# Performance work log

Measured on AMD Instinct MI355X. Metric: run time of the kernel, lower is better.

Reference implementation:

```python
import jax, jax.numpy as jnp
import numpy as np

B, T, H, F, K, NB, MAXL = 32, 512, 512, 512, 3, 256, 2048


def _conv1d(x, w, b, pad):
    # x: [B,T,Cin], w: [K,Cin,Cout] -> [B,T,Cout]
    y = jax.lax.conv_general_dilated(x, w, window_strides=(1,), padding=[(pad, pad)],
                                     dimension_numbers=('NWC', 'WIO', 'NWC'))
    return y + b


def _layernorm(x, g, b):
    m = jnp.mean(x, axis=-1, keepdims=True)
    v = jnp.mean((x - m) ** 2, axis=-1, keepdims=True)
    return (x - m) * jax.lax.rsqrt(v + 1e-5) * g + b


def _variance_predictor(x, mask, cw1, cb1, g1, b1, cw2, cb2, g2, b2, lw, lb, k):
    # ConvNorm(k, pad=(k-1)//2) -> ReLU -> LN -> ConvNorm(k, pad=1) -> ReLU -> LN -> Linear(F,1)
    h = _layernorm(jax.nn.relu(_conv1d(x, cw1, cb1, (k - 1) // 2)), g1, b1)
    h = _layernorm(jax.nn.relu(_conv1d(h, cw2, cb2, 1)), g2, b2)
    out = h @ lw + lb  # [B,T]
    return jnp.where(mask, 0.0, out)


def setup_inputs() -> dict:
    key = jax.random.key(0)
    ks = jax.random.split(key, 12)
    s = 0.02
    inp = {
        'x': jax.random.normal(ks[0], (B, T, H), jnp.float32),
        'src_mask': jnp.zeros((B, T), jnp.bool_),
        'duration': jax.random.randint(ks[1], (B, T), 0, 8),
        'pitch_target': jax.random.normal(ks[2], (B, T), jnp.float32),
        'energy_target': jax.random.normal(ks[3], (B, T), jnp.float32),
        # stacked predictor params: index 0=duration, 1=pitch, 2=energy
        'conv1_w': jax.random.normal(ks[4], (3, K, H, F), jnp.float32) * s,
        'conv1_b': jnp.zeros((3, F), jnp.float32),
        'ln1_g': jnp.ones((3, F), jnp.float32),
        'ln1_b': jnp.zeros((3, F), jnp.float32),
        'conv2_w': jax.random.normal(ks[5], (3, K, F, F), jnp.float32) * s,
        'conv2_b': jnp.zeros((3, F), jnp.float32),
        'ln2_g': jnp.ones((3, F), jnp.float32),
        'ln2_b': jnp.zeros((3, F), jnp.float32),
        'lin_w': jax.random.normal(ks[6], (3, F), jnp.float32) * s,
        'lin_b': jnp.zeros((3,), jnp.float32),
        'pitch_bins': jnp.linspace(-3.0, 3.0, NB - 1, dtype=jnp.float32),
        'energy_bins': jnp.linspace(-3.0, 3.0, NB - 1, dtype=jnp.float32),
        'pitch_table': jax.random.normal(ks[7], (NB, H), jnp.float32) * s,
        'energy_table': jax.random.normal(ks[8], (NB, H), jnp.float32) * s,
        'max_len': MAXL,
    }
    return inp


def reference(x, src_mask, duration, pitch_target, energy_target,
              conv1_w, conv1_b, ln1_g, ln1_b, conv2_w, conv2_b, ln2_g, ln2_b,
              lin_w, lin_b, pitch_bins, energy_bins, pitch_table, energy_table, max_len):
    k = conv1_w.shape[1]

    def vp(i, inp):
        return _variance_predictor(inp, src_mask, conv1_w[i], conv1_b[i], ln1_g[i], ln1_b[i],
                                   conv2_w[i], conv2_b[i], ln2_g[i], ln2_b[i], lin_w[i], lin_b[i], k)

    log_duration_pred = vp(0, x)
    # pitch: predict, bucketize target, add embedding (training path with targets)
    pitch_pred = vp(1, x)
    p_idx = jnp.searchsorted(pitch_bins, pitch_target)  # torch.bucketize
    x = x + pitch_table[p_idx]
    # energy on pitch-conditioned features
    energy_pred = vp(2, x)
    e_idx = jnp.searchsorted(energy_bins, energy_target)
    x = x + energy_table[e_idx]

    # LengthRegulator: expand each phoneme vec duration[b,i] times, pad to max_len
    dur = jnp.where(src_mask, 0, duration)
    cum = jnp.cumsum(dur, axis=1)                 # [B,T]
    mel_len = jnp.minimum(cum[:, -1], max_len)    # [B]
    frames = jnp.arange(max_len)
    idx = jax.vmap(lambda c: jnp.searchsorted(c, frames, side='right'))(cum)
    idx = jnp.clip(idx, 0, x.shape[1] - 1)        # [B,max_len]
    x_out = jnp.take_along_axis(x, idx[:, :, None], axis=1)  # [B,max_len,H]
    mel_mask = frames[None, :] >= mel_len[:, None]
    x_out = jnp.where(mel_mask[:, :, None], 0.0, x_out)
    return x_out, log_duration_pred, pitch_pred, energy_pred, mel_len, mel_mask
```

## Files before the change

kernel.cpp:

```cpp
#include <hip/hip_runtime.h>
#include <hip/hip_bf16.h>

typedef unsigned short ushort_t;
typedef unsigned int uint_t;
typedef __attribute__((ext_vector_type(8))) short bf16x8;
typedef __attribute__((ext_vector_type(4))) float f32x4;

#define NB_T 512
#define NB_B 32
#define NB_M (NB_B * NB_T)
#define KDIM 1536
#define MAXL 2048
#define EPI_STRIDE 144

__device__ __forceinline__ ushort_t f2bf(float f) {
  __hip_bfloat16 h = __float2bfloat16(f);
  return *reinterpret_cast<ushort_t*>(&h);
}
__device__ __forceinline__ float bf2f(ushort_t u) {
  __hip_bfloat16 h;
  *reinterpret_cast<ushort_t*>(&h) = u;
  return __bfloat162float(h);
}
__device__ __forceinline__ uint_t pack2(float a, float b) {
  return (uint_t)f2bf(a) | ((uint_t)f2bf(b) << 16);
}
__device__ __forceinline__ void gload_lds16(const void* g, void* l) {
  __builtin_amdgcn_global_load_lds((const __attribute__((address_space(1))) void*)g,
                                   (__attribute__((address_space(3))) void*)l, 16, 0, 0);
}

__global__ __launch_bounds__(256) void k_wt(const float* __restrict__ w1, const float* __restrict__ w2,
                                            ushort_t* __restrict__ wt1, ushort_t* __restrict__ wt2) {
  __shared__ float tile[64][65];
  int g = blockIdx.y;
  const float* wsrc;
  ushort_t* wdst;
  if (g < 9) { wsrc = w1; wdst = wt1; } else { wsrc = w2; wdst = wt2; g -= 9; }
  const int p = g / 3, kk = g % 3;
  const int ot = (blockIdx.x & 7) * 64;
  const int it = (blockIdx.x >> 3) * 64;
  const int tx = threadIdx.x & 63;
  const int ty = threadIdx.x >> 6;
  const float* src = wsrc + (size_t)g * 512 * 512;
  #pragma unroll
  for (int r = ty; r < 64; r += 4)
    tile[r][tx] = src[(size_t)(it + r) * 512 + ot + tx];
  __syncthreads();
  #pragma unroll
  for (int r = ty; r < 64; r += 4)
    wdst[((size_t)(p * 512 + ot + r)) * KDIM + kk * 512 + it + tx] = f2bf(tile[tx][r]);
}

__global__ __launch_bounds__(512) void k_cum(const int* __restrict__ dur, const unsigned char* __restrict__ mask,
                                             int* __restrict__ cum, float* __restrict__ mel_len_out) {
  __shared__ int s[512];
  const int b = blockIdx.x, t = threadIdx.x;
  int d = mask[b * NB_T + t] ? 0 : dur[b * NB_T + t];
  s[t] = d;
  __syncthreads();
  for (int off = 1; off < 512; off <<= 1) {
    int v = (t >= off) ? s[t - off] : 0;
    __syncthreads();
    s[t] += v;
    __syncthreads();
  }
  cum[b * NB_T + t] = s[t];
  if (t == 0) {
    int ml = s[511]; ml = ml < MAXL ? ml : MAXL;
    mel_len_out[b] = (float)ml;
  }
}

__global__ __launch_bounds__(256) void k_prep(const float* __restrict__ x,
                                              const float* __restrict__ pt, const float* __restrict__ et,
                                              const float* __restrict__ pb, const float* __restrict__ eb,
                                              const float* __restrict__ ptab, const float* __restrict__ etab,
                                              ushort_t* __restrict__ xb_pad, ushort_t* __restrict__ x2pad,
                                              ushort_t* __restrict__ lnp2, ushort_t* __restrict__ x3b) {
  const int rp = blockIdx.x;
  const int b = rp / 514, j = rp % 514;
  const int tid = threadIdx.x;
  if (j == 0 || j == 513) {
    ((uint_t*)(xb_pad + (size_t)rp * 512))[tid] = 0u;
    ((uint_t*)(x2pad + (size_t)rp * 512))[tid] = 0u;
    ((uint_t*)(lnp2 + (size_t)rp * 512))[tid] = 0u;
    return;
  }
  const int m = b * NB_T + j - 1;
  float v = pt[m];
  int lo = 0, hi = 255;
  while (lo < hi) { int mid = (lo + hi) >> 1; if (pb[mid] < v) lo = mid + 1; else hi = mid; }
  const int pi = lo;
  v = et[m]; lo = 0; hi = 255;
  while (lo < hi) { int mid = (lo + hi) >> 1; if (eb[mid] < v) lo = mid + 1; else hi = mid; }
  const int ei = lo;

  const float2 xv = ((const float2*)(x + (size_t)m * 512))[tid];
  const float2 pv = ((const float2*)(ptab + (size_t)pi * 512))[tid];
  const float2 ev = ((const float2*)(etab + (size_t)ei * 512))[tid];
  ((uint_t*)(xb_pad + (size_t)rp * 512))[tid] = pack2(xv.x, xv.y);
  const float ax = xv.x + pv.x, ay = xv.y + pv.y;
  ((uint_t*)(x2pad + (size_t)rp * 512))[tid] = pack2(ax, ay);
  ((uint_t*)(x3b + (size_t)m * 512))[tid] = pack2(ax + ev.x, ay + ev.y);
}

__global__ __launch_bounds__(256) void k_gemm(const ushort_t* __restrict__ A0,
                                              const ushort_t* __restrict__ A1,
                                              const ushort_t* __restrict__ A2,
                                              const ushort_t* __restrict__ Wt,
                                              const float* __restrict__ bias,
                                              ushort_t* __restrict__ H) {
  __shared__ short smem[18432];
  const int tid = threadIdx.x;
  const int lane = tid & 63, wid = tid >> 6;

  const int h = blockIdx.x;
  const int logical = (h & 7) * 192 + (h >> 3);
  const int pred = logical >> 9;
  const int tile = logical & 511;
  const int mt = tile >> 2, nt = tile & 3;
  const int m0 = mt * 128, n0 = nt * 128;
  const int b = m0 >> 9, t0 = m0 & 511;
  const long Arow0 = (long)b * 514 + t0 + 1;

  const ushort_t* Ap = (pred == 0) ? A0 : ((pred == 1) ? A1 : A2);
  const ushort_t* Wp = Wt + (size_t)pred * 512 * KDIM;
  const float* bp = bias + pred * 512;
  ushort_t* Hp = H + (size_t)pred * NB_M * 512;

  const int subr = lane >> 2;
  const int ioff = (lane & 3) * 8;
  const int wr = wid >> 1, wc = wid & 1;
  const int lr = lane & 15, kg = lane >> 4;

  f32x4 acc[4][4];
  #pragma unroll
  for (int i = 0; i < 4; ++i)
    #pragma unroll
    for (int j = 0; j < 4; ++j) acc[i][j] = (f32x4)0.f;

  auto STAGE = [&](int kk, int buf) {
    const int dt = (kk >> 4) - 1;
    const int i0 = (kk & 15) << 5;
    short* la = &smem[buf * 8192];
    short* lb = &smem[buf * 8192 + 4096];
    #pragma unroll
    for (int q = 0; q < 2; ++q) {
      const int chunk = wid * 2 + q;
      const int r = chunk * 16 + subr;
      gload_lds16(Ap + (size_t)(Arow0 + r + dt) * 512 + i0 + ioff, &la[chunk * 512]);
      gload_lds16(Wp + (size_t)(n0 + r) * KDIM + kk * 32 + ioff, &lb[chunk * 512]);
    }
  };

  STAGE(0, 0);
  __syncthreads();
  int buf = 0;
  for (int kk = 0; kk < 48; ++kk) {
    if (kk < 47) STAGE(kk + 1, buf ^ 1);
    const short* la = &smem[buf * 8192];
    const short* lb = &smem[buf * 8192 + 4096];
    bf16x8 af[4], bfv[4];
    #pragma unroll
    for (int fi = 0; fi < 4; ++fi)
      af[fi] = *(const bf16x8*)&la[(wr * 64 + fi * 16 + lr) * 32 + kg * 8];
    #pragma unroll
    for (int fj = 0; fj < 4; ++fj)
      bfv[fj] = *(const bf16x8*)&lb[(wc * 64 + fj * 16 + lr) * 32 + kg * 8];
    #pragma unroll
    for (int fi = 0; fi < 4; ++fi)
      #pragma unroll
      for (int fj = 0; fj < 4; ++fj)
        acc[fi][fj] = __builtin_amdgcn_mfma_f32_16x16x32_bf16(af[fi], bfv[fj], acc[fi][fj], 0, 0, 0);
    __syncthreads();
    buf ^= 1;
  }

  float bvv[4];
  #pragma unroll
  for (int fj = 0; fj < 4; ++fj) bvv[fj] = bp[n0 + wc * 64 + fj * 16 + lr];
  #pragma unroll
  for (int fi = 0; fi < 4; ++fi) {
    const int rowb = wr * 64 + fi * 16 + kg * 4;
    #pragma unroll
    for (int fj = 0; fj < 4; ++fj) {
      const int col = wc * 64 + fj * 16 + lr;
      #pragma unroll
      for (int r = 0; r < 4; ++r) {
        float v = acc[fi][fj][r] + bvv[fj];
        v = v > 0.f ? v : 0.f;
        smem[(rowb + r) * EPI_STRIDE + col] = (short)f2bf(v);
      }
    }
  }
  __syncthreads();
  #pragma unroll
  for (int s = 0; s < 8; ++s) {
    const int chunk = tid + s * 256;
    const int row = chunk >> 4, c8 = (chunk & 15) * 8;
    bf16x8 vv = *(const bf16x8*)&smem[row * EPI_STRIDE + c8];
    *(bf16x8*)(Hp + (size_t)(m0 + row) * 512 + n0 + c8) = vv;
  }
}

__global__ __launch_bounds__(256) void k_ln_mid(const ushort_t* __restrict__ Hh,
                                                const float* __restrict__ g, const float* __restrict__ bb,
                                                ushort_t* __restrict__ lnp0, ushort_t* __restrict__ lnp1,
                                                ushort_t* __restrict__ lnp2) {
  const int rr = blockIdx.x * 4 + (threadIdx.x >> 6);
  const int pred = rr >> 14, m = rr & (NB_M - 1);
  const int lane = threadIdx.x & 63;
  const float* gp = g + pred * 512;
  const float* bp = bb + pred * 512;
  ushort_t* dst = (pred == 0) ? lnp0 : ((pred == 1) ? lnp1 : lnp2);
  bf16x8 v = *(const bf16x8*)(Hh + (size_t)rr * 512 + lane * 8);
  float xv[8];
  float s = 0.f;
  #pragma unroll
  for (int j = 0; j < 8; ++j) { xv[j] = bf2f((ushort_t)v[j]); s += xv[j]; }
  #pragma unroll
  for (int mm = 32; mm >= 1; mm >>= 1) s += __shfl_xor(s, mm, 64);
  const float mean = s * (1.f / 512.f);
  float vs = 0.f;
  #pragma unroll
  for (int j = 0; j < 8; ++j) { float d = xv[j] - mean; vs += d * d; }
  #pragma unroll
  for (int mm = 32; mm >= 1; mm >>= 1) vs += __shfl_xor(vs, mm, 64);
  const float rstd = rsqrtf(vs * (1.f / 512.f) + 1e-5f);
  const float4 g0 = ((const float4*)(gp + lane * 8))[0];
  const float4 g1 = ((const float4*)(gp + lane * 8))[1];
  const float4 b0 = ((const float4*)(bp + lane * 8))[0];
  const float4 b1 = ((const float4*)(bp + lane * 8))[1];
  const float gg[8] = {g0.x, g0.y, g0.z, g0.w, g1.x, g1.y, g1.z, g1.w};
  const float bv[8] = {b0.x, b0.y, b0.z, b0.w, b1.x, b1.y, b1.z, b1.w};
  bf16x8 o;
  #pragma unroll
  for (int j = 0; j < 8; ++j) o[j] = (short)f2bf((xv[j] - mean) * rstd * gg[j] + bv[j]);
  const int bidx = m >> 9, t = m & 511;
  *(bf16x8*)(dst + ((size_t)(bidx * 514 + t + 1)) * 512 + lane * 8) = o;
}

__global__ __launch_bounds__(256) void k_ln_fin(const ushort_t* __restrict__ Hh,
                                                const float* __restrict__ g, const float* __restrict__ bb,
                                                const float* __restrict__ lw, const float* __restrict__ lbp,
                                                const unsigned char* __restrict__ mask,
                                                float* __restrict__ outp) {
  const int rr = blockIdx.x * 4 + (threadIdx.x >> 6);
  const int pred = rr >> 14, m = rr & (NB_M - 1);
  const int lane = threadIdx.x & 63;
  const float* gp = g + pred * 512;
  const float* bp = bb + pred * 512;
  const float* wp = lw + pred * 512;
  bf16x8 v = *(const bf16x8*)(Hh + (size_t)rr * 512 + lane * 8);
  float xv[8];
  float s = 0.f;
  #pragma unroll
  for (int j = 0; j < 8; ++j) { xv[j] = bf2f((ushort_t)v[j]); s += xv[j]; }
  #pragma unroll
  for (int mm = 32; mm >= 1; mm >>= 1) s += __shfl_xor(s, mm, 64);
  const float mean = s * (1.f / 512.f);
  float vs = 0.f;
  #pragma unroll
  for (int j = 0; j < 8; ++j) { float d = xv[j] - mean; vs += d * d; }
  #pragma unroll
  for (int mm = 32; mm >= 1; mm >>= 1) vs += __shfl_xor(vs, mm, 64);
  const float rstd = rsqrtf(vs * (1.f / 512.f) + 1e-5f);
  const float4 g0 = ((const float4*)(gp + lane * 8))[0];
  const float4 g1 = ((const float4*)(gp + lane * 8))[1];
  const float4 b0 = ((const float4*)(bp + lane * 8))[0];
  const float4 b1 = ((const float4*)(bp + lane * 8))[1];
  const float4 w0 = ((const float4*)(wp + lane * 8))[0];
  const float4 w1 = ((const float4*)(wp + lane * 8))[1];
  const float gg[8] = {g0.x, g0.y, g0.z, g0.w, g1.x, g1.y, g1.z, g1.w};
  const float bv[8] = {b0.x, b0.y, b0.z, b0.w, b1.x, b1.y, b1.z, b1.w};
  const float ww[8] = {w0.x, w0.y, w0.z, w0.w, w1.x, w1.y, w1.z, w1.w};
  float dot = 0.f;
  #pragma unroll
  for (int j = 0; j < 8; ++j) dot += ((xv[j] - mean) * rstd * gg[j] + bv[j]) * ww[j];
  #pragma unroll
  for (int mm = 32; mm >= 1; mm >>= 1) dot += __shfl_xor(dot, mm, 64);
  if (lane == 0) {
    float val = dot + lbp[pred];
    if (mask[m]) val = 0.f;
    outp[pred * NB_M + m] = val;
  }
}

__global__ __launch_bounds__(256) void k_regulate(const ushort_t* __restrict__ x3b, const int* __restrict__ cum,
                                                  float* __restrict__ xout, float* __restrict__ mmask) {
  __shared__ int c[512];
  const int blk = blockIdx.x;
  const int b = blk >> 5, chunk = blk & 31;
  const int tid = threadIdx.x, lane = tid & 63, w = tid >> 6;
  c[tid] = cum[b * NB_T + tid];
  c[tid + 256] = cum[b * NB_T + tid + 256];
  __syncthreads();
  int ml = c[511]; ml = ml < MAXL ? ml : MAXL;
  const int f0 = chunk * 64 + w * 16;
  for (int i = 0; i < 16; ++i) {
    const int f = f0 + i;
    float o[8] = {0.f, 0.f, 0.f, 0.f, 0.f, 0.f, 0.f, 0.f};
    if (f < ml) {
      int lo = 0, hi = 512;
      while (lo < hi) { int mid = (lo + hi) >> 1; if (c[mid] <= f) lo = mid + 1; else hi = mid; }
      if (lo > 511) lo = 511;
      bf16x8 vv = *(const bf16x8*)(x3b + ((size_t)(b * NB_T + lo)) * 512 + lane * 8);
      #pragma unroll
      for (int j = 0; j < 8; ++j) o[j] = bf2f((ushort_t)vv[j]);
    }
    float* dst = xout + ((size_t)(b * MAXL + f)) * 512 + lane * 8;
    ((float4*)dst)[0] = make_float4(o[0], o[1], o[2], o[3]);
    ((float4*)dst)[1] = make_float4(o[4], o[5], o[6], o[7]);
    if (lane == 0) mmask[b * MAXL + f] = (f >= ml) ? 1.0f : 0.0f;
  }
}

extern "C" void kernel_launch(void* const* d_in, const int* in_sizes, int n_in,
                              void* d_out, int out_size, void* d_ws, size_t ws_size,
                              hipStream_t stream) {
  const float* x        = (const float*)d_in[0];
  const unsigned char* src_mask = (const unsigned char*)d_in[1];
  const int* duration   = (const int*)d_in[2];
  const float* pitch_t  = (const float*)d_in[3];
  const float* energy_t = (const float*)d_in[4];
  const float* conv1_w  = (const float*)d_in[5];
  const float* conv1_b  = (const float*)d_in[6];
  const float* ln1_g    = (const float*)d_in[7];
  const float* ln1_b    = (const float*)d_in[8];
  const float* conv2_w  = (const float*)d_in[9];
  const float* conv2_b  = (const float*)d_in[10];
  const float* ln2_g    = (const float*)d_in[11];
  const float* ln2_b    = (const float*)d_in[12];
  const float* lin_w    = (const float*)d_in[13];
  const float* lin_b    = (const float*)d_in[14];
  const float* pbins    = (const float*)d_in[15];
  const float* ebins    = (const float*)d_in[16];
  const float* ptab     = (const float*)d_in[17];
  const float* etab     = (const float*)d_in[18];

  char* ws = (char*)d_ws;
  ushort_t* wt1    = (ushort_t*)(ws + 0);
  ushort_t* wt2    = (ushort_t*)(ws + 4718592);
  ushort_t* xb_pad = (ushort_t*)(ws + 9437184);
  ushort_t* x2pad  = (ushort_t*)(ws + 26279936);
  ushort_t* lnp2   = (ushort_t*)(ws + 43122688);
  ushort_t* hbuf   = (ushort_t*)(ws + 59965440);
  ushort_t* x3b    = (ushort_t*)(ws + 110297088);
  int*      cum    = (int*)     (ws + 127074304);

  float* out      = (float*)d_out;
  float* o_xout   = out;
  float* o_preds  = out + 33554432;
  float* o_mellen = o_preds + 3 * NB_M;
  float* o_mmask  = o_mellen + 32;

  k_cum<<<NB_B, 512, 0, stream>>>(duration, src_mask, cum, o_mellen);
  k_wt<<<dim3(64, 18), 256, 0, stream>>>(conv1_w, conv2_w, wt1, wt2);
  k_prep<<<NB_B * 514, 256, 0, stream>>>(x, pitch_t, energy_t, pbins, ebins, ptab, etab,
                                         xb_pad, x2pad, lnp2, x3b);

  k_gemm<<<1536, 256, 0, stream>>>(xb_pad, xb_pad, x2pad, wt1, conv1_b, hbuf);
  k_ln_mid<<<3 * NB_M / 4, 256, 0, stream>>>(hbuf, ln1_g, ln1_b, xb_pad, x2pad, lnp2);
  k_gemm<<<1536, 256, 0, stream>>>(xb_pad, x2pad, lnp2, wt2, conv2_b, hbuf);
  k_ln_fin<<<3 * NB_M / 4, 256, 0, stream>>>(hbuf, ln2_g, ln2_b, lin_w, lin_b, src_mask, o_preds);

  k_regulate<<<1024, 256, 0, stream>>>(x3b, cum, o_xout, o_mmask);
}
```

Measured before the change: 496.0 us.

## Rework conv GEMM to 256x256 tiles with swizzled LDS and phased prefetch

Replaces the 128x128, 4-wave GEMM with 256x256 tiles using 8 waves and 128KB of dynamic LDS, a K-step of 64, and an XOR-swizzled LDS layout to avoid bank conflicts. Prefetch of the next stage is split into four parts interleaved with MFMA phases, using explicit barriers, setprio and vmcnt waits. The epilogue now writes bf16 directly to global instead of staging through LDS. The larger tile is meant to raise operand reuse and MFMA density, at the cost of one block per CU, only 384 blocks, and uncoalesced 2-byte epilogue stores.

Result: no change. 502.6 us (+1.3%).

```diff
diff --git a/kernel.cpp b/kernel.cpp
--- a/kernel.cpp
+++ b/kernel.cpp
@@ -11,7 +11,6 @@
 #define NB_M (NB_B * NB_T)
 #define KDIM 1536
 #define MAXL 2048
-#define EPI_STRIDE 144
 
 __device__ __forceinline__ ushort_t f2bf(float f) {
   __hip_bfloat16 h = __float2bfloat16(f);
@@ -105,22 +104,24 @@
   ((uint_t*)(x3b + (size_t)m * 512))[tid] = pack2(ax + ev.x, ay + ev.y);
 }
 
-__global__ __launch_bounds__(256) void k_gemm(const ushort_t* __restrict__ A0,
-                                              const ushort_t* __restrict__ A1,
-                                              const ushort_t* __restrict__ A2,
-                                              const ushort_t* __restrict__ Wt,
-                                              const float* __restrict__ bias,
-                                              ushort_t* __restrict__ H) {
-  __shared__ short smem[18432];
+__global__ __launch_bounds__(512, 1) void k_gemm(const ushort_t* __restrict__ A0,
+                                                 const ushort_t* __restrict__ A1,
+                                                 const ushort_t* __restrict__ A2,
+                                                 const ushort_t* __restrict__ Wt,
+                                                 const float* __restrict__ bias,
+                                                 ushort_t* __restrict__ H) {
+  extern __shared__ char smem[];
   const int tid = threadIdx.x;
   const int lane = tid & 63, wid = tid >> 6;
-
-  const int h = blockIdx.x;
-  const int logical = (h & 7) * 192 + (h >> 3);
-  const int pred = logical >> 9;
-  const int tile = logical & 511;
-  const int mt = tile >> 2, nt = tile & 3;
-  const int m0 = mt * 128, n0 = nt * 128;
+  const int wr = wid >> 2, wc = wid & 3;
+  const int l15 = lane & 15, l4 = lane >> 4;
+
+  const int bid = blockIdx.x;
+  const int logical = (bid & 7) * 48 + (bid >> 3);
+  const int pred = logical >> 7;
+  const int tl = logical & 127;
+  const int mt = tl >> 1, nt = tl & 1;
+  const int m0 = mt << 8, n0 = nt << 8;
   const int b = m0 >> 9, t0 = m0 & 511;
   const long Arow0 = (long)b * 514 + t0 + 1;
 
@@ -129,78 +130,100 @@
   const float* bp = bias + pred * 512;
   ushort_t* Hp = H + (size_t)pred * NB_M * 512;
 
-  const int subr = lane >> 2;
-  const int ioff = (lane & 3) * 8;
-  const int wr = wid >> 1, wc = wid & 1;
-  const int lr = lane & 15, kg = lane >> 4;
-
-  f32x4 acc[4][4];
-  #pragma unroll
-  for (int i = 0; i < 4; ++i)
+  f32x4 acc[8][4];
+  #pragma unroll
+  for (int i = 0; i < 8; ++i)
     #pragma unroll
     for (int j = 0; j < 4; ++j) acc[i][j] = (f32x4)0.f;
 
-  auto STAGE = [&](int kk, int buf) {
-    const int dt = (kk >> 4) - 1;
-    const int i0 = (kk & 15) << 5;
-    short* la = &smem[buf * 8192];
-    short* lb = &smem[buf * 8192 + 4096];
+  auto STAGE = [&](int jt, int bbuf, int part) {
+    const int h = part & 1;
+    const bool isB = part >= 2;
+    const int tap = jt >> 3;
+    const int kin = (jt & 7) << 6;
     #pragma unroll
     for (int q = 0; q < 2; ++q) {
-      const int chunk = wid * 2 + q;
-      const int r = chunk * 16 + subr;
-      gload_lds16(Ap + (size_t)(Arow0 + r + dt) * 512 + i0 + ioff, &la[chunk * 512]);
-      gload_lds16(Wp + (size_t)(n0 + r) * KDIM + kk * 32 + ioff, &lb[chunk * 512]);
+      const int Ll = q * 8192 + tid * 16;
+      const int Pl = Ll ^ (((Ll >> 9) & 1) << 5);
+      const int row = Pl >> 7;
+      const int kel = (Pl & 127) >> 1;
+      char* ldsb = smem + bbuf * 65536 + (isB ? 32768 : 0) + h * 16384
+                 + q * 8192 + (tid & ~63) * 16;
+      const ushort_t* src;
+      if (isB) src = Wp + (size_t)(n0 + h * 128 + row) * KDIM + jt * 64 + kel;
+      else     src = Ap + (size_t)(Arow0 + h * 128 + row + (tap - 1)) * 512 + kin + kel;
+      gload_lds16(src, ldsb);
     }
   };
-
-  STAGE(0, 0);
-  __syncthreads();
-  int buf = 0;
-  for (int kk = 0; kk < 48; ++kk) {
-    if (kk < 47) STAGE(kk + 1, buf ^ 1);
-    const short* la = &smem[buf * 8192];
-    const short* lb = &smem[buf * 8192 + 4096];
-    bf16x8 af[4], bfv[4];
+  auto LDA = [&](int bbuf, int fr, int ks) -> bf16x8 {
+    const int R = wr * 128 + fr * 16 + l15;
+    const int kb = (ks * 64 + l4 * 16) ^ (((R >> 2) & 1) << 5);
+    return *(const bf16x8*)(smem + bbuf * 65536 + R * 128 + kb);
+  };
+  auto LDB = [&](int bbuf, int fc, int ks) -> bf16x8 {
+    const int R = wc * 64 + fc * 16 + l15;
+    const int kb = (ks * 64 + l4 * 16) ^ (((R >> 2) & 1) << 5);
+    return *(const bf16x8*)(smem + bbuf * 65536 + 32768 + R * 128 + kb);
+  };
+
+  #pragma unroll
+  for (int part = 0; part < 4; ++part) STAGE(0, 0, part);
+  #pragma unroll
+  for (int part = 0; part < 4; ++part) STAGE(1, 1, part);
+  asm volatile("s_waitcnt vmcnt(8)" ::: "memory");
+  __builtin_amdgcn_s_barrier();
+
+  for (int s = 0; s < 24; ++s) {
+    const int bb = s & 1;
+    bf16x8 bF[4][2];
     #pragma unroll
-    for (int fi = 0; fi < 4; ++fi)
-      af[fi] = *(const bf16x8*)&la[(wr * 64 + fi * 16 + lr) * 32 + kg * 8];
+    for (int p = 0; p < 4; ++p) {
+      bf16x8 aF[2][2];
+      #pragma unroll
+      for (int i = 0; i < 2; ++i)
+        #pragma unroll
+        for (int ks = 0; ks < 2; ++ks)
+          aF[i][ks] = LDA(bb, 2 * p + i, ks);
+      if (p == 0) {
+        #pragma unroll
+        for (int fc = 0; fc < 4; ++fc)
+          #pragma unroll
+          for (int ks = 0; ks < 2; ++ks)
+            bF[fc][ks] = LDB(bb, fc, ks);
+      }
+      if (s >= 1 && s <= 22) STAGE(s + 1, bb ^ 1, p);
+      __builtin_amdgcn_s_barrier();
+      __builtin_amdgcn_s_setprio(1);
+      #pragma unroll
+      for (int ks = 0; ks < 2; ++ks)
+        #pragma unroll
+        for (int i = 0; i < 2; ++i)
+          #pragma unroll
+          for (int fc = 0; fc < 4; ++fc)
+            acc[2 * p + i][fc] = __builtin_amdgcn_mfma_f32_16x16x32_bf16(
+                aF[i][ks], bF[fc][ks], acc[2 * p + i][fc], 0, 0, 0);
+      __builtin_amdgcn_s_setprio(0);
+      if (p == 3) asm volatile("s_waitcnt vmcnt(0)" ::: "memory");
+      __builtin_amdgcn_s_barrier();
+    }
+  }
+
+  float bvv[4];
+  #pragma unroll
+  for (int fc = 0; fc < 4; ++fc) bvv[fc] = bp[n0 + wc * 64 + fc * 16 + l15];
+  #pragma unroll
+  for (int fr = 0; fr < 8; ++fr) {
+    const int row0 = m0 + wr * 128 + fr * 16 + l4 * 4;
     #pragma unroll
-    for (int fj = 0; fj < 4; ++fj)
-      bfv[fj] = *(const bf16x8*)&lb[(wc * 64 + fj * 16 + lr) * 32 + kg * 8];
-    #pragma unroll
-    for (int fi = 0; fi < 4; ++fi)
-      #pragma unroll
-      for (int fj = 0; fj < 4; ++fj)
-        acc[fi][fj] = __builtin_amdgcn_mfma_f32_16x16x32_bf16(af[fi], bfv[fj], acc[fi][fj], 0, 0, 0);
-    __syncthreads();
-    buf ^= 1;
-  }
-
-  float bvv[4];
-  #pragma unroll
-  for (int fj = 0; fj < 4; ++fj) bvv[fj] = bp[n0 + wc * 64 + fj * 16 + lr];
-  #pragma unroll
-  for (int fi = 0; fi < 4; ++fi) {
-    const int rowb = wr * 64 + fi * 16 + kg * 4;
-    #pragma unroll
-    for (int fj = 0; fj < 4; ++fj) {
-      const int col = wc * 64 + fj * 16 + lr;
+    for (int fc = 0; fc < 4; ++fc) {
+      const int col = n0 + wc * 64 + fc * 16 + l15;
       #pragma unroll
       for (int r = 0; r < 4; ++r) {
-        float v = acc[fi][fj][r] + bvv[fj];
+        float v = acc[fr][fc][r] + bvv[fc];
         v = v > 0.f ? v : 0.f;
-        smem[(rowb + r) * EPI_STRIDE + col] = (short)f2bf(v);
+        Hp[(size_t)(row0 + r) * 512 + col] = f2bf(v);
       }
     }
-  }
-  __syncthreads();
-  #pragma unroll
-  for (int s = 0; s < 8; ++s) {
-    const int chunk = tid + s * 256;
-    const int row = chunk >> 4, c8 = (chunk & 15) * 8;
-    bf16x8 vv = *(const bf16x8*)&smem[row * EPI_STRIDE + c8];
-    *(bf16x8*)(Hp + (size_t)(m0 + row) * 512 + n0 + c8) = vv;
   }
 }
 
@@ -360,9 +383,9 @@
   k_prep<<<NB_B * 514, 256, 0, stream>>>(x, pitch_t, energy_t, pbins, ebins, ptab, etab,
                                          xb_pad, x2pad, lnp2, x3b);
 
-  k_gemm<<<1536, 256, 0, stream>>>(xb_pad, xb_pad, x2pad, wt1, conv1_b, hbuf);
+  k_gemm<<<384, 512, 131072, stream>>>(xb_pad, xb_pad, x2pad, wt1, conv1_b, hbuf);
   k_ln_mid<<<3 * NB_M / 4, 256, 0, stream>>>(hbuf, ln1_g, ln1_b, xb_pad, x2pad, lnp2);
-  k_gemm<<<1536, 256, 0, stream>>>(xb_pad, x2pad, lnp2, wt2, conv2_b, hbuf);
+  k_gemm<<<384, 512, 131072, stream>>>(xb_pad, x2pad, lnp2, wt2, conv2_b, hbuf);
   k_ln_fin<<<3 * NB_M / 4, 256, 0, stream>>>(hbuf, ln2_g, ln2_b, lin_w, lin_b, src_mask, o_preds);
 
   k_regulate<<<1024, 256, 0, stream>>>(x3b, cum, o_xout, o_mmask);
```
